# Kernel optimization log

Hardware: AMD Instinct MI355X
Metric: run time of the kernel (lower is better)

The kernel has to match this reference:

```python
import jax, jax.numpy as jnp
import numpy as np

# LLaMA-7B FFN dims; batch split evenly across A adapters (the batch-sliced loop
# in the torch module becomes a vectorized per-adapter leading axis here).
D = 4096      # d_model
H = 11008     # ffn hidden
A = 4         # number of adapters (batch slices)
B = 8         # total batch (sequences); B % A == 0
S = 512       # seq len
R = 16        # LoRA rank
EPS = 1e-5


def setup_inputs() -> dict:
    key = jax.random.key(0)
    ks = jax.random.split(key, 11)
    g = lambda k, shape, sc: (jax.random.normal(k, shape, dtype=jnp.float32) * sc)
    return {
        "data": g(ks[0], (B, S, D), 1.0),
        "norm_w": jnp.ones((D,), jnp.float32),
        "W1": g(ks[1], (D, H), 0.02),
        "W3": g(ks[2], (D, H), 0.02),
        "W2": g(ks[3], (H, D), 0.02),
        # per-adapter LoRA factors for w1, w3, w2
        "A1": g(ks[4], (A, D, R), 0.02), "B1": g(ks[5], (A, R, H), 0.02),
        "A3": g(ks[6], (A, D, R), 0.02), "B3": g(ks[7], (A, R, H), 0.02),
        "A2": g(ks[8], (A, H, R), 0.02), "B2": g(ks[9], (A, R, D), 0.02),
    }


def reference(data, norm_w, W1, W3, W2, A1, B1, A3, B3, A2, B2):
    # RMSNorm
    inv = jax.lax.rsqrt(jnp.mean(data * data, axis=-1, keepdims=True) + EPS)
    x = data * inv * norm_w                     # [B, S, D]
    # view batch as [A, B//A, S, D]: each adapter owns a contiguous batch slice
    xa = x.reshape(A, B // A, S, D)
    # w1 / w3 with per-adapter low-rank LoRA additions
    h1 = jnp.einsum("absd,dh->absh", xa, W1) + jnp.einsum(
        "absr,arh->absh", jnp.einsum("absd,adr->absr", xa, A1), B1)
    h3 = jnp.einsum("absd,dh->absh", xa, W3) + jnp.einsum(
        "absr,arh->absh", jnp.einsum("absd,adr->absr", xa, A3), B3)
    act = jax.nn.silu(h1) * h3                  # [A, B//A, S, H]
    out = jnp.einsum("absh,hd->absd", act, W2) + jnp.einsum(
        "absr,ard->absd", jnp.einsum("absh,ahr->absr", act, A2), B2)
    # concat of adapter slices == reshape back
    return out.reshape(B, S, D)
```

## Files before the change

### kernel.cpp

```cpp
#include <hip/hip_runtime.h>
#include <stdint.h>

#define DD 4096
#define HH 11008
#define RANK 16
#define NTOK 4096

typedef __attribute__((ext_vector_type(8))) short short8;
typedef __attribute__((ext_vector_type(4))) float f32x4;

static __device__ __forceinline__ unsigned short f2bf(float f) {
    union { float f; uint32_t u; } x; x.f = f;
    uint32_t r = (x.u + 0x7fffu + ((x.u >> 16) & 1u)) >> 16;
    return (unsigned short)r;
}
static __device__ __forceinline__ float bf2f(unsigned short s) {
    union { uint32_t u; float f; } x; x.u = ((uint32_t)s) << 16;
    return x.f;
}

static __device__ __forceinline__ void gl_lds16(const unsigned short* g, unsigned short* l) {
    __builtin_amdgcn_global_load_lds(
        (const __attribute__((address_space(1))) unsigned int*)g,
        (__attribute__((address_space(3))) unsigned int*)l, 16, 0, 0);
}

__global__ __launch_bounds__(256) void rmsnorm_kernel(
    const float* __restrict__ data, const float* __restrict__ nw,
    unsigned short* __restrict__ xb) {
    const int row = blockIdx.x;
    const int t = threadIdx.x;
    const float4* dr = (const float4*)(data + (size_t)row * DD);
    float4 v[4];
    float ss = 0.f;
#pragma unroll
    for (int i = 0; i < 4; i++) {
        v[i] = dr[t + 256 * i];
        ss += v[i].x * v[i].x + v[i].y * v[i].y + v[i].z * v[i].z + v[i].w * v[i].w;
    }
#pragma unroll
    for (int off = 32; off > 0; off >>= 1) ss += __shfl_down(ss, off);
    __shared__ float red[4];
    if ((t & 63) == 0) red[t >> 6] = ss;
    __syncthreads();
    float total = red[0] + red[1] + red[2] + red[3];
    float inv = rsqrtf(total / (float)DD + 1e-5f);
    const float4* wr = (const float4*)nw;
    uint2* xo = (uint2*)(xb + (size_t)row * DD);
#pragma unroll
    for (int i = 0; i < 4; i++) {
        float4 w = wr[t + 256 * i];
        union { unsigned short u[4]; uint2 q; } p;
        p.u[0] = f2bf(v[i].x * inv * w.x);
        p.u[1] = f2bf(v[i].y * inv * w.y);
        p.u[2] = f2bf(v[i].z * inv * w.z);
        p.u[3] = f2bf(v[i].w * inv * w.w);
        xo[t + 256 * i] = p.q;
    }
}

__global__ __launch_bounds__(256) void transpose_cvt(
    const float* __restrict__ W, unsigned short* __restrict__ WT, int K, int N) {
    __shared__ float tile[64][65];
    const int t = threadIdx.x;
    const int n0 = blockIdx.x * 64, k0 = blockIdx.y * 64;
    const int cn = (t & 15) * 4, rk = t >> 4;
#pragma unroll
    for (int p = 0; p < 4; p++) {
        int kk = rk + p * 16;
        float4 v = *(const float4*)(W + (size_t)(k0 + kk) * N + n0 + cn);
        tile[kk][cn] = v.x; tile[kk][cn + 1] = v.y;
        tile[kk][cn + 2] = v.z; tile[kk][cn + 3] = v.w;
    }
    __syncthreads();
    const int n = t >> 2, ks = (t & 3) * 16;
    union { unsigned short u[16]; uint4 q[2]; } pk;
#pragma unroll
    for (int j = 0; j < 16; j++) pk.u[j] = f2bf(tile[ks + j][n]);
    uint4* dst = (uint4*)(WT + (size_t)(n0 + n) * K + k0 + ks);
    dst[0] = pk.q[0];
    dst[1] = pk.q[1];
}

__global__ __launch_bounds__(256) void lora_x_kernel(
    const unsigned short* __restrict__ xb, const float* __restrict__ A1,
    const float* __restrict__ A3, float* __restrict__ t1, float* __restrict__ t3) {
    const int row0 = blockIdx.x * 16;
    const int a = row0 >> 10;
    const int t = threadIdx.x;
    const int tok = t >> 4, rk = t & 15;
    __shared__ unsigned short xs[16][264];
    __shared__ float a1s[256][16];
    __shared__ float a3s[256][16];
    float acc1 = 0.f, acc3 = 0.f;
    for (int c = 0; c < DD / 256; c++) {
        const int d0 = c * 256;
        __syncthreads();
#pragma unroll
        for (int i = 0; i < 2; i++) {
            int idx = t + 256 * i;
            int r = idx >> 5, cs = (idx & 31) * 8;
            *(uint4*)&xs[r][cs] = *(const uint4*)(xb + (size_t)(row0 + r) * DD + d0 + cs);
        }
        const float* A1c = A1 + ((size_t)a * DD + d0) * RANK;
        const float* A3c = A3 + ((size_t)a * DD + d0) * RANK;
#pragma unroll
        for (int i = 0; i < 4; i++) {
            int j = (t + 256 * i) * 4;
            *(float4*)&((float*)a1s)[j] = *(const float4*)(A1c + j);
            *(float4*)&((float*)a3s)[j] = *(const float4*)(A3c + j);
        }
        __syncthreads();
#pragma unroll 8
        for (int d = 0; d < 256; d++) {
            float xv = bf2f(xs[tok][d]);
            acc1 += xv * a1s[d][rk];
            acc3 += xv * a3s[d][rk];
        }
    }
    t1[(size_t)(row0 + tok) * RANK + rk] = acc1;
    t3[(size_t)(row0 + tok) * RANK + rk] = acc3;
}

__global__ __launch_bounds__(256) void lora_act_kernel(
    const unsigned short* __restrict__ act, const float* __restrict__ A2,
    float* __restrict__ t2) {
    const int row0 = blockIdx.x * 16;
    const int a = row0 >> 10;
    const int t = threadIdx.x;
    const int tok = t >> 4, rk = t & 15;
    __shared__ unsigned short xs[16][264];
    __shared__ float a2s[256][16];
    float acc = 0.f;
    for (int c = 0; c < HH / 256; c++) {
        const int d0 = c * 256;
        __syncthreads();
#pragma unroll
        for (int i = 0; i < 2; i++) {
            int idx = t + 256 * i;
            int r = idx >> 5, cs = (idx & 31) * 8;
            *(uint4*)&xs[r][cs] = *(const uint4*)(act + (size_t)(row0 + r) * HH + d0 + cs);
        }
        const float* A2c = A2 + ((size_t)a * HH + d0) * RANK;
#pragma unroll
        for (int i = 0; i < 4; i++) {
            int j = (t + 256 * i) * 4;
            *(float4*)&((float*)a2s)[j] = *(const float4*)(A2c + j);
        }
        __syncthreads();
#pragma unroll 8
        for (int d = 0; d < 256; d++) {
            acc += bf2f(xs[tok][d]) * a2s[d][rk];
        }
    }
    t2[(size_t)(row0 + tok) * RANK + rk] = acc;
}

__global__ __launch_bounds__(256, 3) void gemm1_kernel(
    const unsigned short* __restrict__ xb, const unsigned short* __restrict__ W1T,
    const unsigned short* __restrict__ W3T, const float* __restrict__ t1,
    const float* __restrict__ t3, const float* __restrict__ B1f,
    const float* __restrict__ B3f, unsigned short* __restrict__ act) {
    const int m0 = blockIdx.x * 128, n0 = blockIdx.y * 128;
    const int a = m0 >> 10;
    const int t = threadIdx.x;
    const int lane = t & 63, w = t >> 6, wm = w & 1, wn = w >> 1;
    const int lr = lane & 15, q = lane >> 4;
    const int srow = lane >> 2;
    const int scol = (lane & 3) * 8;
    __shared__ __align__(16) unsigned short Al[128 * 32];
    __shared__ __align__(16) unsigned short B1l[128 * 32];
    __shared__ __align__(16) unsigned short B3l[128 * 32];
    f32x4 acc1[4][4], acc3[4][4];
#pragma unroll
    for (int mi = 0; mi < 4; mi++)
#pragma unroll
        for (int nj = 0; nj < 4; nj++) {
            acc1[mi][nj] = (f32x4){0.f, 0.f, 0.f, 0.f};
            acc3[mi][nj] = (f32x4){0.f, 0.f, 0.f, 0.f};
        }

    const unsigned short* gA  = xb  + (size_t)(m0 + w * 32 + srow) * DD + scol;
    const unsigned short* gB1 = W1T + (size_t)(n0 + w * 32 + srow) * DD + scol;
    const unsigned short* gB3 = W3T + (size_t)(n0 + w * 32 + srow) * DD + scol;
    unsigned short* lA  = &Al[w * 1024];
    unsigned short* lB1 = &B1l[w * 1024];
    unsigned short* lB3 = &B3l[w * 1024];

    for (int kt = 0; kt < DD / 32; kt++) {
        const int kof = kt * 32;
        gl_lds16(gA  + kof,                    lA);
        gl_lds16(gA  + kof + (size_t)16 * DD,  lA + 512);
        gl_lds16(gB1 + kof,                    lB1);
        gl_lds16(gB1 + kof + (size_t)16 * DD,  lB1 + 512);
        gl_lds16(gB3 + kof,                    lB3);
        gl_lds16(gB3 + kof + (size_t)16 * DD,  lB3 + 512);
        __syncthreads();
        short8 av[4];
#pragma unroll
        for (int mi = 0; mi < 4; mi++)
            av[mi] = *reinterpret_cast<const short8*>(&Al[(wm * 64 + mi * 16 + lr) * 32 + q * 8]);
#pragma unroll
        for (int nj = 0; nj < 4; nj++) {
            short8 b1 = *reinterpret_cast<const short8*>(&B1l[(wn * 64 + nj * 16 + lr) * 32 + q * 8]);
            short8 b3 = *reinterpret_cast<const short8*>(&B3l[(wn * 64 + nj * 16 + lr) * 32 + q * 8]);
#pragma unroll
            for (int mi = 0; mi < 4; mi++) {
                acc1[mi][nj] = __builtin_amdgcn_mfma_f32_16x16x32_bf16(av[mi], b1, acc1[mi][nj], 0, 0, 0);
                acc3[mi][nj] = __builtin_amdgcn_mfma_f32_16x16x32_bf16(av[mi], b3, acc3[mi][nj], 0, 0, 0);
            }
        }
        __syncthreads();
    }

    {
        const int arow = t >> 1, hf = t & 1;
        uint4 z; z.x = z.y = z.z = z.w = 0u;
        const float4* tp = (const float4*)(t1 + (size_t)(m0 + arow) * RANK + hf * 8);
        float4 u0 = tp[0], u1 = tp[1];
        union { unsigned short u[8]; uint4 q; } pa;
        pa.u[0] = f2bf(u0.x); pa.u[1] = f2bf(u0.y); pa.u[2] = f2bf(u0.z); pa.u[3] = f2bf(u0.w);
        pa.u[4] = f2bf(u1.x); pa.u[5] = f2bf(u1.y); pa.u[6] = f2bf(u1.z); pa.u[7] = f2bf(u1.w);
        *(uint4*)&Al[arow * 32 + hf * 8] = pa.q;
        *(uint4*)&Al[arow * 32 + 16 + hf * 8] = z;
        union { unsigned short u[8]; uint4 q; } pb;
#pragma unroll
        for (int j = 0; j < 8; j++)
            pb.u[j] = f2bf(B1f[((size_t)a * RANK + hf * 8 + j) * HH + n0 + arow]);
        *(uint4*)&B1l[arow * 32 + hf * 8] = pb.q;
        *(uint4*)&B1l[arow * 32 + 16 + hf * 8] = z;
        __syncthreads();
        short8 av[4];
#pragma unroll
        for (int mi = 0; mi < 4; mi++)
            av[mi] = *reinterpret_cast<const short8*>(&Al[(wm * 64 + mi * 16 + lr) * 32 + q * 8]);
#pragma unroll
        for (int nj = 0; nj < 4; nj++) {
            short8 b1 = *reinterpret_cast<const short8*>(&B1l[(wn * 64 + nj * 16 + lr) * 32 + q * 8]);
#pragma unroll
            for (int mi = 0; mi < 4; mi++)
                acc1[mi][nj] = __builtin_amdgcn_mfma_f32_16x16x32_bf16(av[mi], b1, acc1[mi][nj], 0, 0, 0);
        }
        __syncthreads();
        const float4* tp3 = (const float4*)(t3 + (size_t)(m0 + arow) * RANK + hf * 8);
        float4 w0 = tp3[0], w1 = tp3[1];
        pa.u[0] = f2bf(w0.x); pa.u[1] = f2bf(w0.y); pa.u[2] = f2bf(w0.z); pa.u[3] = f2bf(w0.w);
        pa.u[4] = f2bf(w1.x); pa.u[5] = f2bf(w1.y); pa.u[6] = f2bf(w1.z); pa.u[7] = f2bf(w1.w);
        *(uint4*)&Al[arow * 32 + hf * 8] = pa.q;
        *(uint4*)&Al[arow * 32 + 16 + hf * 8] = z;
#pragma unroll
        for (int j = 0; j < 8; j++)
            pb.u[j] = f2bf(B3f[((size_t)a * RANK + hf * 8 + j) * HH + n0 + arow]);
        *(uint4*)&B3l[arow * 32 + hf * 8] = pb.q;
        *(uint4*)&B3l[arow * 32 + 16 + hf * 8] = z;
        __syncthreads();
#pragma unroll
        for (int mi = 0; mi < 4; mi++)
            av[mi] = *reinterpret_cast<const short8*>(&Al[(wm * 64 + mi * 16 + lr) * 32 + q * 8]);
#pragma unroll
        for (int nj = 0; nj < 4; nj++) {
            short8 b3 = *reinterpret_cast<const short8*>(&B3l[(wn * 64 + nj * 16 + lr) * 32 + q * 8]);
#pragma unroll
            for (int mi = 0; mi < 4; mi++)
                acc3[mi][nj] = __builtin_amdgcn_mfma_f32_16x16x32_bf16(av[mi], b3, acc3[mi][nj], 0, 0, 0);
        }
    }

#pragma unroll
    for (int mi = 0; mi < 4; mi++)
#pragma unroll
        for (int nj = 0; nj < 4; nj++)
#pragma unroll
            for (int rg = 0; rg < 4; rg++) {
                int row = wm * 64 + mi * 16 + q * 4 + rg;
                int col = wn * 64 + nj * 16 + lr;
                float h1 = acc1[mi][nj][rg];
                float h3 = acc3[mi][nj][rg];
                float sig = 1.f / (1.f + __expf(-h1));
                float o = h1 * sig * h3;
                act[(size_t)(m0 + row) * HH + n0 + col] = f2bf(o);
            }
}

__global__ __launch_bounds__(256, 3) void gemm2_kernel(
    const unsigned short* __restrict__ actb, const unsigned short* __restrict__ W2T,
    const float* __restrict__ t2, const float* __restrict__ B2f,
    float* __restrict__ out) {
    const int m0 = blockIdx.x * 128, n0 = blockIdx.y * 128;
    const int a = m0 >> 10;
    const int t = threadIdx.x;
    const int lane = t & 63, w = t >> 6, wm = w & 1, wn = w >> 1;
    const int lr = lane & 15, q = lane >> 4;
    const int srow = lane >> 2;
    const int scol = (lane & 3) * 8;
    __shared__ __align__(16) unsigned short Al[128 * 32];
    __shared__ __align__(16) unsigned short Bl[128 * 32];
    f32x4 acc[4][4];
#pragma unroll
    for (int mi = 0; mi < 4; mi++)
#pragma unroll
        for (int nj = 0; nj < 4; nj++) acc[mi][nj] = (f32x4){0.f, 0.f, 0.f, 0.f};

    const unsigned short* gA = actb + (size_t)(m0 + w * 32 + srow) * HH + scol;
    const unsigned short* gB = W2T  + (size_t)(n0 + w * 32 + srow) * HH + scol;
    unsigned short* lA = &Al[w * 1024];
    unsigned short* lB = &Bl[w * 1024];

    for (int kt = 0; kt < HH / 32; kt++) {
        const int kof = kt * 32;
        gl_lds16(gA + kof,                   lA);
        gl_lds16(gA + kof + (size_t)16 * HH, lA + 512);
        gl_lds16(gB + kof,                   lB);
        gl_lds16(gB + kof + (size_t)16 * HH, lB + 512);
        __syncthreads();
        short8 av[4];
#pragma unroll
        for (int mi = 0; mi < 4; mi++)
            av[mi] = *reinterpret_cast<const short8*>(&Al[(wm * 64 + mi * 16 + lr) * 32 + q * 8]);
#pragma unroll
        for (int nj = 0; nj < 4; nj++) {
            short8 b = *reinterpret_cast<const short8*>(&Bl[(wn * 64 + nj * 16 + lr) * 32 + q * 8]);
#pragma unroll
            for (int mi = 0; mi < 4; mi++)
                acc[mi][nj] = __builtin_amdgcn_mfma_f32_16x16x32_bf16(av[mi], b, acc[mi][nj], 0, 0, 0);
        }
        __syncthreads();
    }

    {
        const int arow = t >> 1, hf = t & 1;
        uint4 z; z.x = z.y = z.z = z.w = 0u;
        const float4* tp = (const float4*)(t2 + (size_t)(m0 + arow) * RANK + hf * 8);
        float4 u0 = tp[0], u1 = tp[1];
        union { unsigned short u[8]; uint4 q; } pa;
        pa.u[0] = f2bf(u0.x); pa.u[1] = f2bf(u0.y); pa.u[2] = f2bf(u0.z); pa.u[3] = f2bf(u0.w);
        pa.u[4] = f2bf(u1.x); pa.u[5] = f2bf(u1.y); pa.u[6] = f2bf(u1.z); pa.u[7] = f2bf(u1.w);
        *(uint4*)&Al[arow * 32 + hf * 8] = pa.q;
        *(uint4*)&Al[arow * 32 + 16 + hf * 8] = z;
        union { unsigned short u[8]; uint4 q; } pb;
#pragma unroll
        for (int j = 0; j < 8; j++)
            pb.u[j] = f2bf(B2f[((size_t)a * RANK + hf * 8 + j) * DD + n0 + arow]);
        *(uint4*)&Bl[arow * 32 + hf * 8] = pb.q;
        *(uint4*)&Bl[arow * 32 + 16 + hf * 8] = z;
        __syncthreads();
        short8 av[4];
#pragma unroll
        for (int mi = 0; mi < 4; mi++)
            av[mi] = *reinterpret_cast<const short8*>(&Al[(wm * 64 + mi * 16 + lr) * 32 + q * 8]);
#pragma unroll
        for (int nj = 0; nj < 4; nj++) {
            short8 b = *reinterpret_cast<const short8*>(&Bl[(wn * 64 + nj * 16 + lr) * 32 + q * 8]);
#pragma unroll
            for (int mi = 0; mi < 4; mi++)
                acc[mi][nj] = __builtin_amdgcn_mfma_f32_16x16x32_bf16(av[mi], b, acc[mi][nj], 0, 0, 0);
        }
    }

#pragma unroll
    for (int mi = 0; mi < 4; mi++)
#pragma unroll
        for (int nj = 0; nj < 4; nj++)
#pragma unroll
            for (int rg = 0; rg < 4; rg++) {
                int row = wm * 64 + mi * 16 + q * 4 + rg;
                int col = wn * 64 + nj * 16 + lr;
                out[(size_t)(m0 + row) * DD + n0 + col] = acc[mi][nj][rg];
            }
}

extern "C" void kernel_launch(void* const* d_in, const int* in_sizes, int n_in,
                              void* d_out, int out_size, void* d_ws, size_t ws_size,
                              hipStream_t stream) {
    const float* data = (const float*)d_in[0];
    const float* norm_w = (const float*)d_in[1];
    const float* W1 = (const float*)d_in[2];
    const float* W3 = (const float*)d_in[3];
    const float* W2 = (const float*)d_in[4];
    const float* A1 = (const float*)d_in[5];
    const float* B1 = (const float*)d_in[6];
    const float* A3 = (const float*)d_in[7];
    const float* B3 = (const float*)d_in[8];
    const float* A2 = (const float*)d_in[9];
    const float* B2 = (const float*)d_in[10];
    float* out = (float*)d_out;

    char* ws = (char*)d_ws;
    const size_t WT_BYTES = (size_t)DD * HH * 2;
    unsigned short* W1T = (unsigned short*)(ws + 0);
    unsigned short* W3T = (unsigned short*)(ws + WT_BYTES);
    unsigned short* W2T = (unsigned short*)(ws + 0);
    unsigned short* xb  = (unsigned short*)(ws + 2 * WT_BYTES);
    unsigned short* act = (unsigned short*)(ws + 2 * WT_BYTES + (size_t)NTOK * DD * 2);
    float* t1 = (float*)(ws + 2 * WT_BYTES + (size_t)NTOK * DD * 2 + (size_t)NTOK * HH * 2);
    float* t3 = t1 + (size_t)NTOK * RANK;
    float* t2 = t3 + (size_t)NTOK * RANK;

    rmsnorm_kernel<<<NTOK, 256, 0, stream>>>(data, norm_w, xb);
    transpose_cvt<<<dim3(HH / 64, DD / 64), 256, 0, stream>>>(W1, W1T, DD, HH);
    transpose_cvt<<<dim3(HH / 64, DD / 64), 256, 0, stream>>>(W3, W3T, DD, HH);
    lora_x_kernel<<<NTOK / 16, 256, 0, stream>>>(xb, A1, A3, t1, t3);
    gemm1_kernel<<<dim3(32, HH / 128), 256, 0, stream>>>(xb, W1T, W3T, t1, t3, B1, B3, act);
    transpose_cvt<<<dim3(DD / 64, HH / 64), 256, 0, stream>>>(W2, W2T, HH, DD);
    lora_act_kernel<<<NTOK / 16, 256, 0, stream>>>(act, A2, t2);
    gemm2_kernel<<<dim3(32, DD / 128), 256, 0, stream>>>(act, W2T, t2, B2, out);
}
```

Baseline: 2.054 ms.

## Rewrite both GEMMs with 256-row tiles, double-buffered swizzled LDS pipeline

Both main GEMM kernels move to 512-thread workgroups with 256x128 (gemm1) and 256x256 (gemm2) tiles. They use a 64-wide K step with XOR-swizzled LDS layouts and double-buffered global-to-LDS prefetch, interleaving loads with MFMA phases under explicit waitcnt, barriers and s_setprio. Blocks are remapped so that groups of consecutive workgroups are spread across XCDs. The intent is to hide memory latency, cut LDS bank conflicts and increase reuse per tile, at the cost of more registers and LDS and lower occupancy.

```diff
diff --git a/kernel.cpp b/kernel.cpp
--- a/kernel.cpp
+++ b/kernel.cpp
@@ -24,6 +24,16 @@
         (const __attribute__((address_space(1))) unsigned int*)g,
         (__attribute__((address_space(3))) unsigned int*)l, 16, 0, 0);
 }
+
+static __device__ __forceinline__ void barx() {
+    __builtin_amdgcn_sched_barrier(0);
+    __builtin_amdgcn_s_barrier();
+    __builtin_amdgcn_sched_barrier(0);
+}
+#define VMW(n) do { asm volatile("s_waitcnt vmcnt(" #n ")" ::: "memory"); } while (0)
+#define LGW0() do { asm volatile("s_waitcnt lgkmcnt(0)" ::: "memory"); __builtin_amdgcn_sched_barrier(0); } while (0)
+#define PRIO1() __builtin_amdgcn_s_setprio(1)
+#define PRIO0() __builtin_amdgcn_s_setprio(0)
 
 __global__ __launch_bounds__(256) void rmsnorm_kernel(
     const float* __restrict__ data, const float* __restrict__ nw,
@@ -156,217 +166,331 @@
     t2[(size_t)(row0 + tok) * RANK + rk] = acc;
 }
 
-__global__ __launch_bounds__(256, 3) void gemm1_kernel(
+__global__ __launch_bounds__(512, 2) void gemm1_kernel(
     const unsigned short* __restrict__ xb, const unsigned short* __restrict__ W1T,
     const unsigned short* __restrict__ W3T, const float* __restrict__ t1,
     const float* __restrict__ t3, const float* __restrict__ B1f,
     const float* __restrict__ B3f, unsigned short* __restrict__ act) {
-    const int m0 = blockIdx.x * 128, n0 = blockIdx.y * 128;
+    const int nwg = gridDim.x;
+    const int cpx = nwg >> 3;
+    const int bid = blockIdx.x;
+    const int wg = (bid & 7) * cpx + (bid >> 3);
+    const int NTN = HH / 128;
+    const int m0 = (wg / NTN) * 256;
+    const int n0 = (wg % NTN) * 128;
     const int a = m0 >> 10;
     const int t = threadIdx.x;
-    const int lane = t & 63, w = t >> 6, wm = w & 1, wn = w >> 1;
+    const int w = t >> 6, lane = t & 63;
+    const int wm = w & 1, wn = w >> 1;
     const int lr = lane & 15, q = lane >> 4;
-    const int srow = lane >> 2;
-    const int scol = (lane & 3) * 8;
-    __shared__ __align__(16) unsigned short Al[128 * 32];
-    __shared__ __align__(16) unsigned short B1l[128 * 32];
-    __shared__ __align__(16) unsigned short B3l[128 * 32];
-    f32x4 acc1[4][4], acc3[4][4];
-#pragma unroll
-    for (int mi = 0; mi < 4; mi++)
-#pragma unroll
-        for (int nj = 0; nj < 4; nj++) {
+    const int lrow = lane >> 3;
+    const int lcol = ((lane & 7) ^ lrow) * 8;
+
+    __shared__ __align__(16) unsigned short lds[65536];
+    unsigned short* LA  = lds;
+    unsigned short* LB1 = lds + 32768;
+    unsigned short* LB3 = lds + 49152;
+
+    const unsigned short* gA  = xb  + (size_t)(m0 + lrow) * DD + lcol;
+    const unsigned short* gB1 = W1T + (size_t)(n0 + lrow) * DD + lcol;
+    const unsigned short* gB3 = W3T + (size_t)(n0 + lrow) * DD + lcol;
+
+#define STG1(gp, lp) do { \
+    gl_lds16((gp) + (size_t)(w * 8) * DD,      (lp) + w * 512); \
+    gl_lds16((gp) + (size_t)(64 + w * 8) * DD, (lp) + 4096 + w * 512); } while (0)
+
+    f32x4 acc1[8][2], acc3[8][2];
+#pragma unroll
+    for (int mi = 0; mi < 8; mi++)
+#pragma unroll
+        for (int nj = 0; nj < 2; nj++) {
             acc1[mi][nj] = (f32x4){0.f, 0.f, 0.f, 0.f};
             acc3[mi][nj] = (f32x4){0.f, 0.f, 0.f, 0.f};
         }
-
-    const unsigned short* gA  = xb  + (size_t)(m0 + w * 32 + srow) * DD + scol;
-    const unsigned short* gB1 = W1T + (size_t)(n0 + w * 32 + srow) * DD + scol;
-    const unsigned short* gB3 = W3T + (size_t)(n0 + w * 32 + srow) * DD + scol;
-    unsigned short* lA  = &Al[w * 1024];
-    unsigned short* lB1 = &B1l[w * 1024];
-    unsigned short* lB3 = &B3l[w * 1024];
-
-    for (int kt = 0; kt < DD / 32; kt++) {
-        const int kof = kt * 32;
-        gl_lds16(gA  + kof,                    lA);
-        gl_lds16(gA  + kof + (size_t)16 * DD,  lA + 512);
-        gl_lds16(gB1 + kof,                    lB1);
-        gl_lds16(gB1 + kof + (size_t)16 * DD,  lB1 + 512);
-        gl_lds16(gB3 + kof,                    lB3);
-        gl_lds16(gB3 + kof + (size_t)16 * DD,  lB3 + 512);
-        __syncthreads();
-        short8 av[4];
-#pragma unroll
-        for (int mi = 0; mi < 4; mi++)
-            av[mi] = *reinterpret_cast<const short8*>(&Al[(wm * 64 + mi * 16 + lr) * 32 + q * 8]);
-#pragma unroll
-        for (int nj = 0; nj < 4; nj++) {
-            short8 b1 = *reinterpret_cast<const short8*>(&B1l[(wn * 64 + nj * 16 + lr) * 32 + q * 8]);
-            short8 b3 = *reinterpret_cast<const short8*>(&B3l[(wn * 64 + nj * 16 + lr) * 32 + q * 8]);
-#pragma unroll
-            for (int mi = 0; mi < 4; mi++) {
-                acc1[mi][nj] = __builtin_amdgcn_mfma_f32_16x16x32_bf16(av[mi], b1, acc1[mi][nj], 0, 0, 0);
-                acc3[mi][nj] = __builtin_amdgcn_mfma_f32_16x16x32_bf16(av[mi], b3, acc3[mi][nj], 0, 0, 0);
-            }
-        }
-        __syncthreads();
-    }
+    short8 av[4], b1r[2][2], b3r[2][2];
+
+#define RDA1(d, h, kk) do { _Pragma("unroll") \
+    for (int mi = 0; mi < 4; mi++) { int rw = wm * 128 + (h) * 64 + mi * 16 + lr; \
+        av[mi] = *reinterpret_cast<const short8*>( \
+            &LA[(d) * 16384 + rw * 64 + (((kk) * 32 + q * 8) ^ ((rw & 7) << 3))]); } } while (0)
+#define RDB1(d, kk) do { _Pragma("unroll") \
+    for (int nj = 0; nj < 2; nj++) { int rw = wn * 32 + nj * 16 + lr; \
+        int co = rw * 64 + (((kk) * 32 + q * 8) ^ ((rw & 7) << 3)); \
+        b1r[kk][nj] = *reinterpret_cast<const short8*>(&LB1[(d) * 8192 + co]); \
+        b3r[kk][nj] = *reinterpret_cast<const short8*>(&LB3[(d) * 8192 + co]); } } while (0)
+#define MM1(h, kk) do { _Pragma("unroll") \
+    for (int nj = 0; nj < 2; nj++) { _Pragma("unroll") \
+        for (int mi = 0; mi < 4; mi++) { \
+            acc1[(h) * 4 + mi][nj] = __builtin_amdgcn_mfma_f32_16x16x32_bf16( \
+                av[mi], b1r[kk][nj], acc1[(h) * 4 + mi][nj], 0, 0, 0); \
+            acc3[(h) * 4 + mi][nj] = __builtin_amdgcn_mfma_f32_16x16x32_bf16( \
+                av[mi], b3r[kk][nj], acc3[(h) * 4 + mi][nj], 0, 0, 0); } } } while (0)
+
+    STG1(gA, LA);
+    STG1(gA + (size_t)128 * DD, LA + 8192);
+    STG1(gB1, LB1);
+    STG1(gB3, LB3);
+    STG1(gB1 + 64, LB1 + 8192);
+    STG1(gB3 + 64, LB3 + 8192);
+    VMW(4); barx();
+
+    const int NT = DD / 64;
+#pragma unroll 1
+    for (int it = 0; it < NT / 2; ++it) {
+        const int O = 2 * it + 1;
+        const int Kc = (2 * it + 2 < NT) ? 2 * it + 2 : NT - 1;
+        const int Oc = (2 * it + 3 < NT) ? 2 * it + 3 : NT - 1;
+        RDA1(0, 0, 0); RDB1(0, 0);
+        STG1(gA + (size_t)O * 64, LA + 16384);
+        barx(); LGW0(); PRIO1(); MM1(0, 0); PRIO0(); barx();
+        RDA1(0, 0, 1); RDB1(0, 1);
+        STG1(gA + (size_t)O * 64 + (size_t)128 * DD, LA + 16384 + 8192);
+        barx(); LGW0(); PRIO1(); MM1(0, 1); PRIO0(); barx();
+        RDA1(0, 1, 0);
+        STG1(gB1 + (size_t)Kc * 64, LB1);
+        barx(); LGW0(); PRIO1(); MM1(1, 0); PRIO0(); barx();
+        RDA1(0, 1, 1);
+        STG1(gB3 + (size_t)Kc * 64, LB3);
+        barx(); LGW0(); PRIO1(); MM1(1, 1); PRIO0(); VMW(4); barx();
+        RDA1(1, 0, 0); RDB1(1, 0);
+        STG1(gA + (size_t)Kc * 64, LA);
+        barx(); LGW0(); PRIO1(); MM1(0, 0); PRIO0(); barx();
+        RDA1(1, 0, 1); RDB1(1, 1);
+        STG1(gA + (size_t)Kc * 64 + (size_t)128 * DD, LA + 8192);
+        barx(); LGW0(); PRIO1(); MM1(0, 1); PRIO0(); barx();
+        RDA1(1, 1, 0);
+        STG1(gB1 + (size_t)Oc * 64, LB1 + 8192);
+        barx(); LGW0(); PRIO1(); MM1(1, 0); PRIO0(); barx();
+        RDA1(1, 1, 1);
+        STG1(gB3 + (size_t)Oc * 64, LB3 + 8192);
+        barx(); LGW0(); PRIO1(); MM1(1, 1); PRIO0(); VMW(4); barx();
+    }
+
+    VMW(0); barx();
 
     {
         const int arow = t >> 1, hf = t & 1;
         uint4 z; z.x = z.y = z.z = z.w = 0u;
-        const float4* tp = (const float4*)(t1 + (size_t)(m0 + arow) * RANK + hf * 8);
-        float4 u0 = tp[0], u1 = tp[1];
-        union { unsigned short u[8]; uint4 q; } pa;
+        const int sw = (arow & 7) << 3;
+        const float4* tp1 = (const float4*)(t1 + (size_t)(m0 + arow) * RANK + hf * 8);
+        float4 u0 = tp1[0], u1 = tp1[1];
+        union { unsigned short u[8]; uint4 qv; } pa;
         pa.u[0] = f2bf(u0.x); pa.u[1] = f2bf(u0.y); pa.u[2] = f2bf(u0.z); pa.u[3] = f2bf(u0.w);
         pa.u[4] = f2bf(u1.x); pa.u[5] = f2bf(u1.y); pa.u[6] = f2bf(u1.z); pa.u[7] = f2bf(u1.w);
-        *(uint4*)&Al[arow * 32 + hf * 8] = pa.q;
-        *(uint4*)&Al[arow * 32 + 16 + hf * 8] = z;
-        union { unsigned short u[8]; uint4 q; } pb;
+        *(uint4*)&LA[arow * 64 + ((hf * 8) ^ sw)] = pa.qv;
+        *(uint4*)&LA[arow * 64 + ((16 + hf * 8) ^ sw)] = z;
+        const float4* tp3 = (const float4*)(t3 + (size_t)(m0 + arow) * RANK + hf * 8);
+        float4 v0 = tp3[0], v1 = tp3[1];
+        pa.u[0] = f2bf(v0.x); pa.u[1] = f2bf(v0.y); pa.u[2] = f2bf(v0.z); pa.u[3] = f2bf(v0.w);
+        pa.u[4] = f2bf(v1.x); pa.u[5] = f2bf(v1.y); pa.u[6] = f2bf(v1.z); pa.u[7] = f2bf(v1.w);
+        *(uint4*)&LA[16384 + arow * 64 + ((hf * 8) ^ sw)] = pa.qv;
+        *(uint4*)&LA[16384 + arow * 64 + ((16 + hf * 8) ^ sw)] = z;
+        const int n = (t & 255) >> 1;
+        const float* Bsrc = (t < 256) ? B1f : B3f;
+        unsigned short* Ldst = (t < 256) ? LB1 : LB3;
+        union { unsigned short u[8]; uint4 qv; } pb;
 #pragma unroll
         for (int j = 0; j < 8; j++)
-            pb.u[j] = f2bf(B1f[((size_t)a * RANK + hf * 8 + j) * HH + n0 + arow]);
-        *(uint4*)&B1l[arow * 32 + hf * 8] = pb.q;
-        *(uint4*)&B1l[arow * 32 + 16 + hf * 8] = z;
-        __syncthreads();
-        short8 av[4];
-#pragma unroll
-        for (int mi = 0; mi < 4; mi++)
-            av[mi] = *reinterpret_cast<const short8*>(&Al[(wm * 64 + mi * 16 + lr) * 32 + q * 8]);
-#pragma unroll
-        for (int nj = 0; nj < 4; nj++) {
-            short8 b1 = *reinterpret_cast<const short8*>(&B1l[(wn * 64 + nj * 16 + lr) * 32 + q * 8]);
-#pragma unroll
-            for (int mi = 0; mi < 4; mi++)
-                acc1[mi][nj] = __builtin_amdgcn_mfma_f32_16x16x32_bf16(av[mi], b1, acc1[mi][nj], 0, 0, 0);
-        }
-        __syncthreads();
-        const float4* tp3 = (const float4*)(t3 + (size_t)(m0 + arow) * RANK + hf * 8);
-        float4 w0 = tp3[0], w1 = tp3[1];
-        pa.u[0] = f2bf(w0.x); pa.u[1] = f2bf(w0.y); pa.u[2] = f2bf(w0.z); pa.u[3] = f2bf(w0.w);
-        pa.u[4] = f2bf(w1.x); pa.u[5] = f2bf(w1.y); pa.u[6] = f2bf(w1.z); pa.u[7] = f2bf(w1.w);
-        *(uint4*)&Al[arow * 32 + hf * 8] = pa.q;
-        *(uint4*)&Al[arow * 32 + 16 + hf * 8] = z;
-#pragma unroll
-        for (int j = 0; j < 8; j++)
-            pb.u[j] = f2bf(B3f[((size_t)a * RANK + hf * 8 + j) * HH + n0 + arow]);
-        *(uint4*)&B3l[arow * 32 + hf * 8] = pb.q;
-        *(uint4*)&B3l[arow * 32 + 16 + hf * 8] = z;
-        __syncthreads();
-#pragma unroll
-        for (int mi = 0; mi < 4; mi++)
-            av[mi] = *reinterpret_cast<const short8*>(&Al[(wm * 64 + mi * 16 + lr) * 32 + q * 8]);
-#pragma unroll
-        for (int nj = 0; nj < 4; nj++) {
-            short8 b3 = *reinterpret_cast<const short8*>(&B3l[(wn * 64 + nj * 16 + lr) * 32 + q * 8]);
-#pragma unroll
-            for (int mi = 0; mi < 4; mi++)
-                acc3[mi][nj] = __builtin_amdgcn_mfma_f32_16x16x32_bf16(av[mi], b3, acc3[mi][nj], 0, 0, 0);
-        }
-    }
-
-#pragma unroll
-    for (int mi = 0; mi < 4; mi++)
-#pragma unroll
-        for (int nj = 0; nj < 4; nj++)
+            pb.u[j] = f2bf(Bsrc[((size_t)a * RANK + hf * 8 + j) * HH + n0 + n]);
+        const int swn = (n & 7) << 3;
+        *(uint4*)&Ldst[n * 64 + ((hf * 8) ^ swn)] = pb.qv;
+        *(uint4*)&Ldst[n * 64 + ((16 + hf * 8) ^ swn)] = z;
+    }
+    __syncthreads();
+    {
+        short8 la[8];
+#pragma unroll
+        for (int mi = 0; mi < 8; mi++) {
+            int rw = wm * 128 + mi * 16 + lr;
+            la[mi] = *reinterpret_cast<const short8*>(&LA[rw * 64 + ((q * 8) ^ ((rw & 7) << 3))]);
+        }
+#pragma unroll
+        for (int nj = 0; nj < 2; nj++) {
+            int rw = wn * 32 + nj * 16 + lr;
+            short8 b1 = *reinterpret_cast<const short8*>(&LB1[rw * 64 + ((q * 8) ^ ((rw & 7) << 3))]);
+#pragma unroll
+            for (int mi = 0; mi < 8; mi++)
+                acc1[mi][nj] = __builtin_amdgcn_mfma_f32_16x16x32_bf16(la[mi], b1, acc1[mi][nj], 0, 0, 0);
+        }
+#pragma unroll
+        for (int mi = 0; mi < 8; mi++) {
+            int rw = wm * 128 + mi * 16 + lr;
+            la[mi] = *reinterpret_cast<const short8*>(&LA[16384 + rw * 64 + ((q * 8) ^ ((rw & 7) << 3))]);
+        }
+#pragma unroll
+        for (int nj = 0; nj < 2; nj++) {
+            int rw = wn * 32 + nj * 16 + lr;
+            short8 b3 = *reinterpret_cast<const short8*>(&LB3[rw * 64 + ((q * 8) ^ ((rw & 7) << 3))]);
+#pragma unroll
+            for (int mi = 0; mi < 8; mi++)
+                acc3[mi][nj] = __builtin_amdgcn_mfma_f32_16x16x32_bf16(la[mi], b3, acc3[mi][nj], 0, 0, 0);
+        }
+    }
+
+#pragma unroll
+    for (int mi = 0; mi < 8; mi++)
+#pragma unroll
+        for (int nj = 0; nj < 2; nj++)
 #pragma unroll
             for (int rg = 0; rg < 4; rg++) {
-                int row = wm * 64 + mi * 16 + q * 4 + rg;
-                int col = wn * 64 + nj * 16 + lr;
+                int row = wm * 128 + mi * 16 + q * 4 + rg;
+                int col = wn * 32 + nj * 16 + lr;
                 float h1 = acc1[mi][nj][rg];
                 float h3 = acc3[mi][nj][rg];
                 float sig = 1.f / (1.f + __expf(-h1));
-                float o = h1 * sig * h3;
-                act[(size_t)(m0 + row) * HH + n0 + col] = f2bf(o);
+                act[(size_t)(m0 + row) * HH + n0 + col] = f2bf(h1 * sig * h3);
             }
-}
-
-__global__ __launch_bounds__(256, 3) void gemm2_kernel(
+#undef STG1
+#undef RDA1
+#undef RDB1
+#undef MM1
+}
+
+__global__ __launch_bounds__(512, 2) void gemm2_kernel(
     const unsigned short* __restrict__ actb, const unsigned short* __restrict__ W2T,
     const float* __restrict__ t2, const float* __restrict__ B2f,
     float* __restrict__ out) {
-    const int m0 = blockIdx.x * 128, n0 = blockIdx.y * 128;
+    const int nwg = gridDim.x;
+    const int cpx = nwg >> 3;
+    const int bid = blockIdx.x;
+    const int wg = (bid & 7) * cpx + (bid >> 3);
+    const int NTN = DD / 256;
+    const int m0 = (wg / NTN) * 256;
+    const int n0 = (wg % NTN) * 256;
     const int a = m0 >> 10;
     const int t = threadIdx.x;
-    const int lane = t & 63, w = t >> 6, wm = w & 1, wn = w >> 1;
+    const int w = t >> 6, lane = t & 63;
+    const int wm = w & 1, wn = w >> 1;
     const int lr = lane & 15, q = lane >> 4;
-    const int srow = lane >> 2;
-    const int scol = (lane & 3) * 8;
-    __shared__ __align__(16) unsigned short Al[128 * 32];
-    __shared__ __align__(16) unsigned short Bl[128 * 32];
-    f32x4 acc[4][4];
-#pragma unroll
-    for (int mi = 0; mi < 4; mi++)
+    const int lrow = lane >> 3;
+    const int lcol = ((lane & 7) ^ lrow) * 8;
+
+    __shared__ __align__(16) unsigned short lds[65536];
+    unsigned short* LA = lds;
+    unsigned short* LB = lds + 32768;
+
+    const unsigned short* gA = actb + (size_t)(m0 + lrow) * HH + lcol;
+    const unsigned short* gB = W2T  + (size_t)(n0 + lrow) * HH + lcol;
+
+#define STG2(gp, lp) do { \
+    gl_lds16((gp) + (size_t)(w * 8) * HH,      (lp) + w * 512); \
+    gl_lds16((gp) + (size_t)(64 + w * 8) * HH, (lp) + 4096 + w * 512); } while (0)
+
+    f32x4 acc[8][4];
+#pragma unroll
+    for (int mi = 0; mi < 8; mi++)
 #pragma unroll
         for (int nj = 0; nj < 4; nj++) acc[mi][nj] = (f32x4){0.f, 0.f, 0.f, 0.f};
-
-    const unsigned short* gA = actb + (size_t)(m0 + w * 32 + srow) * HH + scol;
-    const unsigned short* gB = W2T  + (size_t)(n0 + w * 32 + srow) * HH + scol;
-    unsigned short* lA = &Al[w * 1024];
-    unsigned short* lB = &Bl[w * 1024];
-
-    for (int kt = 0; kt < HH / 32; kt++) {
-        const int kof = kt * 32;
-        gl_lds16(gA + kof,                   lA);
-        gl_lds16(gA + kof + (size_t)16 * HH, lA + 512);
-        gl_lds16(gB + kof,                   lB);
-        gl_lds16(gB + kof + (size_t)16 * HH, lB + 512);
-        __syncthreads();
-        short8 av[4];
-#pragma unroll
-        for (int mi = 0; mi < 4; mi++)
-            av[mi] = *reinterpret_cast<const short8*>(&Al[(wm * 64 + mi * 16 + lr) * 32 + q * 8]);
-#pragma unroll
-        for (int nj = 0; nj < 4; nj++) {
-            short8 b = *reinterpret_cast<const short8*>(&Bl[(wn * 64 + nj * 16 + lr) * 32 + q * 8]);
-#pragma unroll
-            for (int mi = 0; mi < 4; mi++)
-                acc[mi][nj] = __builtin_amdgcn_mfma_f32_16x16x32_bf16(av[mi], b, acc[mi][nj], 0, 0, 0);
-        }
-        __syncthreads();
-    }
+    short8 av[4], br[2][4];
+
+#define RDA2(d, h, kk) do { _Pragma("unroll") \
+    for (int mi = 0; mi < 4; mi++) { int rw = wm * 128 + (h) * 64 + mi * 16 + lr; \
+        av[mi] = *reinterpret_cast<const short8*>( \
+            &LA[(d) * 16384 + rw * 64 + (((kk) * 32 + q * 8) ^ ((rw & 7) << 3))]); } } while (0)
+#define RDB2(d, kk) do { _Pragma("unroll") \
+    for (int nj = 0; nj < 4; nj++) { int rw = wn * 64 + nj * 16 + lr; \
+        br[kk][nj] = *reinterpret_cast<const short8*>( \
+            &LB[(d) * 16384 + rw * 64 + (((kk) * 32 + q * 8) ^ ((rw & 7) << 3))]); } } while (0)
+#define MM2(h, kk) do { _Pragma("unroll") \
+    for (int nj = 0; nj < 4; nj++) { _Pragma("unroll") \
+        for (int mi = 0; mi < 4; mi++) { \
+            acc[(h) * 4 + mi][nj] = __builtin_amdgcn_mfma_f32_16x16x32_bf16( \
+                av[mi], br[kk][nj], acc[(h) * 4 + mi][nj], 0, 0, 0); } } } while (0)
+
+    STG2(gA, LA);
+    STG2(gA + (size_t)128 * HH, LA + 8192);
+    STG2(gB, LB);
+    STG2(gB + (size_t)128 * HH, LB + 8192);
+    STG2(gB + 64, LB + 16384);
+    STG2(gB + 64 + (size_t)128 * HH, LB + 16384 + 8192);
+    VMW(4); barx();
+
+    const int NT = HH / 64;
+#pragma unroll 1
+    for (int it = 0; it < NT / 2; ++it) {
+        const int O = 2 * it + 1;
+        const int Kc = (2 * it + 2 < NT) ? 2 * it + 2 : NT - 1;
+        const int Oc = (2 * it + 3 < NT) ? 2 * it + 3 : NT - 1;
+        RDA2(0, 0, 0); RDB2(0, 0);
+        STG2(gA + (size_t)O * 64, LA + 16384);
+        barx(); LGW0(); PRIO1(); MM2(0, 0); PRIO0(); barx();
+        RDA2(0, 0, 1); RDB2(0, 1);
+        STG2(gA + (size_t)O * 64 + (size_t)128 * HH, LA + 16384 + 8192);
+        barx(); LGW0(); PRIO1(); MM2(0, 1); PRIO0(); barx();
+        RDA2(0, 1, 0);
+        STG2(gB + (size_t)Kc * 64, LB);
+        barx(); LGW0(); PRIO1(); MM2(1, 0); PRIO0(); barx();
+        RDA2(0, 1, 1);
+        STG2(gB + (size_t)Kc * 64 + (size_t)128 * HH, LB + 8192);
+        barx(); LGW0(); PRIO1(); MM2(1, 1); PRIO0(); VMW(4); barx();
+        RDA2(1, 0, 0); RDB2(1, 0);
+        STG2(gA + (size_t)Kc * 64, LA);
+        barx(); LGW0(); PRIO1(); MM2(0, 0); PRIO0(); barx();
+        RDA2(1, 0, 1); RDB2(1, 1);
+        STG2(gA + (size_t)Kc * 64 + (size_t)128 * HH, LA + 8192);
+        barx(); LGW0(); PRIO1(); MM2(0, 1); PRIO0(); barx();
+        RDA2(1, 1, 0);
+        STG2(gB + (size_t)Oc * 64, LB + 16384);
+        barx(); LGW0(); PRIO1(); MM2(1, 0); PRIO0(); barx();
+        RDA2(1, 1, 1);
+        STG2(gB + (size_t)Oc * 64 + (size_t)128 * HH, LB + 16384 + 8192);
+        barx(); LGW0(); PRIO1(); MM2(1, 1); PRIO0(); VMW(4); barx();
+    }
+
+    VMW(0); barx();
 
     {
         const int arow = t >> 1, hf = t & 1;
         uint4 z; z.x = z.y = z.z = z.w = 0u;
+        const int sw = (arow & 7) << 3;
         const float4* tp = (const float4*)(t2 + (size_t)(m0 + arow) * RANK + hf * 8);
         float4 u0 = tp[0], u1 = tp[1];
-        union { unsigned short u[8]; uint4 q; } pa;
+        union { unsigned short u[8]; uint4 qv; } pa;
         pa.u[0] = f2bf(u0.x); pa.u[1] = f2bf(u0.y); pa.u[2] = f2bf(u0.z); pa.u[3] = f2bf(u0.w);
         pa.u[4] = f2bf(u1.x); pa.u[5] = f2bf(u1.y); pa.u[6] = f2bf(u1.z); pa.u[7] = f2bf(u1.w);
-        *(uint4*)&Al[arow * 32 + hf * 8] = pa.q;
-        *(uint4*)&Al[arow * 32 + 16 + hf * 8] = z;
-        union { unsigned short u[8]; uint4 q; } pb;
+        *(uint4*)&LA[arow * 64 + ((hf * 8) ^ sw)] = pa.qv;
+        *(uint4*)&LA[arow * 64 + ((16 + hf * 8) ^ sw)] = z;
+        const int n = t >> 1;
+        union { unsigned short u[8]; uint4 qv; } pb;
 #pragma unroll
         for (int j = 0; j < 8; j++)
-            pb.u[j] = f2bf(B2f[((size_t)a * RANK + hf * 8 + j) * DD + n0 + arow]);
-        *(uint4*)&Bl[arow * 32 + hf * 8] = pb.q;
-        *(uint4*)&Bl[arow * 32 + 16 + hf * 8] = z;
-        __syncthreads();
-        short8 av[4];
-#pragma unroll
-        for (int mi = 0; mi < 4; mi++)
-            av[mi] = *reinterpret_cast<const short8*>(&Al[(wm * 64 + mi * 16 + lr) * 32 + q * 8]);
+            pb.u[j] = f2bf(B2f[((size_t)a * RANK + hf * 8 + j) * DD + n0 + n]);
+        const int swn = (n & 7) << 3;
+        *(uint4*)&LB[n * 64 + ((hf * 8) ^ swn)] = pb.qv;
+        *(uint4*)&LB[n * 64 + ((16 + hf * 8) ^ swn)] = z;
+    }
+    __syncthreads();
+    {
+        short8 la[8];
+#pragma unroll
+        for (int mi = 0; mi < 8; mi++) {
+            int rw = wm * 128 + mi * 16 + lr;
+            la[mi] = *reinterpret_cast<const short8*>(&LA[rw * 64 + ((q * 8) ^ ((rw & 7) << 3))]);
+        }
 #pragma unroll
         for (int nj = 0; nj < 4; nj++) {
-            short8 b = *reinterpret_cast<const short8*>(&Bl[(wn * 64 + nj * 16 + lr) * 32 + q * 8]);
-#pragma unroll
-            for (int mi = 0; mi < 4; mi++)
-                acc[mi][nj] = __builtin_amdgcn_mfma_f32_16x16x32_bf16(av[mi], b, acc[mi][nj], 0, 0, 0);
-        }
-    }
-
-#pragma unroll
-    for (int mi = 0; mi < 4; mi++)
+            int rw = wn * 64 + nj * 16 + lr;
+            short8 b = *reinterpret_cast<const short8*>(&LB[rw * 64 + ((q * 8) ^ ((rw & 7) << 3))]);
+#pragma unroll
+            for (int mi = 0; mi < 8; mi++)
+                acc[mi][nj] = __builtin_amdgcn_mfma_f32_16x16x32_bf16(la[mi], b, acc[mi][nj], 0, 0, 0);
+        }
+    }
+
+#pragma unroll
+    for (int mi = 0; mi < 8; mi++)
 #pragma unroll
         for (int nj = 0; nj < 4; nj++)
 #pragma unroll
             for (int rg = 0; rg < 4; rg++) {
-                int row = wm * 64 + mi * 16 + q * 4 + rg;
+                int row = wm * 128 + mi * 16 + q * 4 + rg;
                 int col = wn * 64 + nj * 16 + lr;
                 out[(size_t)(m0 + row) * DD + n0 + col] = acc[mi][nj][rg];
             }
+#undef STG2
+#undef RDA2
+#undef RDB2
+#undef MM2
 }
 
 extern "C" void kernel_launch(void* const* d_in, const int* in_sizes, int n_in,
@@ -400,8 +524,8 @@
     transpose_cvt<<<dim3(HH / 64, DD / 64), 256, 0, stream>>>(W1, W1T, DD, HH);
     transpose_cvt<<<dim3(HH / 64, DD / 64), 256, 0, stream>>>(W3, W3T, DD, HH);
     lora_x_kernel<<<NTOK / 16, 256, 0, stream>>>(xb, A1, A3, t1, t3);
-    gemm1_kernel<<<dim3(32, HH / 128), 256, 0, stream>>>(xb, W1T, W3T, t1, t3, B1, B3, act);
+    gemm1_kernel<<<dim3((NTOK / 256) * (HH / 128)), 512, 0, stream>>>(xb, W1T, W3T, t1, t3, B1, B3, act);
     transpose_cvt<<<dim3(DD / 64, HH / 64), 256, 0, stream>>>(W2, W2T, HH, DD);
     lora_act_kernel<<<NTOK / 16, 256, 0, stream>>>(act, A2, t2);
-    gemm2_kernel<<<dim3(32, DD / 128), 256, 0, stream>>>(act, W2T, t2, B2, out);
-}
+    gemm2_kernel<<<dim3((NTOK / 256) * (DD / 256)), 512, 0, stream>>>(act, W2T, t2, B2, out);
+}
```

Result: faster. 1.706 ms (-17.0%).
